# Kernel optimization log

Hardware: AMD Instinct MI355X
Metric: run time of the kernel (lower is better)

The kernel has to match this reference:

```python
import jax, jax.numpy as jnp
import numpy as np

L_XYZ = 10  # fourier freqs for position -> 3 + 6*10 = 63 dims
L_DIR = 4   # fourier freqs for direction -> 3 + 6*4 = 27 dims
DIM = 32    # radiance feature dim per depth layer
PPP = 4     # points (depth layers) per pixel
HID = 128   # MLP hidden width
UCH = 64    # UNet hidden channels


def pe(x, L):
    # fourier positional encoding: [x, sin(2^k x), cos(2^k x)]
    f = (2.0 ** jnp.arange(L)).astype(x.dtype)
    xf = x[..., None] * f  # [..., 3, L]
    s = jnp.sin(xf).reshape(x.shape[:-1] + (-1,))
    c = jnp.cos(xf).reshape(x.shape[:-1] + (-1,))
    return jnp.concatenate([x, s, c], axis=-1)


def conv(x, w, b):
    y = jax.lax.conv_general_dilated(x, w, (1, 1), 'SAME',
                                     dimension_numbers=('NCHW', 'OIHW', 'NCHW'))
    return y + b[None, :, None, None]


def setup_inputs() -> dict:
    key = jax.random.key(0)
    ks = jax.random.split(key, 24)
    H = W = 384
    zbufs = jax.random.uniform(ks[0], (H, W, PPP), dtype=jnp.float32)  # depths in [0,1)
    o = jax.random.normal(ks[1], (H, W, 3), dtype=jnp.float32)
    d = jax.random.normal(ks[2], (H, W, 3), dtype=jnp.float32)
    d = d / jnp.linalg.norm(d, axis=-1, keepdims=True)
    cos = jax.random.uniform(ks[3], (H, W, 1), dtype=jnp.float32) * 0.5 + 0.5
    ray = jnp.concatenate([o, d, cos], axis=-1)  # [H,W,7]
    gt = jax.random.uniform(ks[4], (H, W, 3), dtype=jnp.float32)
    mask_gt = jnp.ones((H, W, 1), dtype=jnp.float32)
    xyz_o = jax.random.normal(ks[5], (1024, 3), dtype=jnp.float32)
    in_xyz = 3 + 6 * L_XYZ
    in_dir = 3 + 6 * L_DIR
    in_ch = DIM * PPP
    p = {}
    p['w1'] = jax.random.normal(ks[6], (in_xyz, HID), dtype=jnp.float32) * 0.05
    p['b1'] = jnp.zeros((HID,), dtype=jnp.float32)
    p['w2'] = jax.random.normal(ks[7], (HID, HID), dtype=jnp.float32) * 0.05
    p['b2'] = jnp.zeros((HID,), dtype=jnp.float32)
    p['w3'] = jax.random.normal(ks[8], (HID + in_dir, DIM), dtype=jnp.float32) * 0.05
    p['b3'] = jnp.zeros((DIM,), dtype=jnp.float32)
    p['mpn_w1'] = jax.random.normal(ks[9], (in_ch, in_ch, 3, 3), dtype=jnp.float32) * 0.02
    p['mpn_b1'] = jnp.zeros((in_ch,), dtype=jnp.float32)
    p['mpn_w2'] = jax.random.normal(ks[10], (in_ch, in_ch, 3, 3), dtype=jnp.float32) * 0.02
    p['mpn_b2'] = jnp.zeros((in_ch,), dtype=jnp.float32)
    p['uw1'] = jax.random.normal(ks[11], (UCH, in_ch, 3, 3), dtype=jnp.float32) * 0.02
    p['ub1'] = jnp.zeros((UCH,), dtype=jnp.float32)
    p['uw2'] = jax.random.normal(ks[12], (UCH, UCH, 3, 3), dtype=jnp.float32) * 0.02
    p['ub2'] = jnp.zeros((UCH,), dtype=jnp.float32)
    p['uw3'] = jax.random.normal(ks[13], (3, UCH, 3, 3), dtype=jnp.float32) * 0.02
    p['ub3'] = jnp.zeros((3,), dtype=jnp.float32)
    inp = {'zbufs': zbufs, 'ray': ray, 'gt': gt, 'mask_gt': mask_gt,
           'isTrain': 1, 'xyz_o': xyz_o}
    inp.update(p)
    return inp


def reference(zbufs, ray, gt, mask_gt, isTrain, xyz_o,
              w1, b1, w2, b2, w3, b3,
              mpn_w1, mpn_b1, mpn_w2, mpn_b2,
              uw1, ub1, uw2, ub2, uw3, ub3):
    H, W, P = zbufs.shape
    o = ray[..., :3]
    dirs = ray[..., 3:6]
    cos = ray[..., 6:7]
    thresh = 0.2 if isTrain else 0.0
    # dense equivalent of boolean-mask gather -> MLP -> scatter into zeros
    mask = (zbufs > thresh).astype(zbufs.dtype)  # [H,W,P]
    # xyz_near = o + dirs * zbuf / cos  (xyznear path)
    xyz = o[..., None, :] + dirs[..., None, :] * zbufs[..., None] / cos[..., None]  # [H,W,P,3]
    x = pe(xyz, L_XYZ)                                   # [H,W,P,63]
    h = jax.nn.relu(x @ w1 + b1)                         # [H,W,P,HID]
    h = jax.nn.relu(h @ w2 + b2)
    dpe = pe(dirs, L_DIR)                                # [H,W,27]
    dpe = jnp.broadcast_to(dpe[..., None, :], h.shape[:-1] + (dpe.shape[-1],))
    feat = jnp.concatenate([h, dpe], axis=-1) @ w3 + b3  # [H,W,P,DIM]
    feat = feat * mask[..., None]                        # zeros where pix_mask is False
    # per-layer permute(2,3,0,1) + cat(dim=1) == [1, P*DIM, H, W]
    rdmp = feat.transpose(2, 3, 0, 1).reshape(1, P * DIM, H, W)
    # MPN: predicted per-channel mask
    m = jax.nn.sigmoid(conv(jax.nn.relu(conv(rdmp, mpn_w1, mpn_b1)), mpn_w2, mpn_b2))
    fuse = rdmp * m
    fea_map = jax.nn.sigmoid(fuse[0, :3].transpose(1, 2, 0))  # [H,W,3]
    # UNet refinement to RGB
    u = jax.nn.relu(conv(fuse, uw1, ub1))
    u = jax.nn.relu(conv(u, uw2, ub2))
    img = jax.nn.sigmoid(conv(u, uw3, ub3))[0].transpose(1, 2, 0)  # [H,W,3]
    return img
```

## Files before the change

kernel.cpp:

```cpp
#include <hip/hip_runtime.h>
#include <hip/hip_bf16.h>
#include <math.h>

typedef __attribute__((ext_vector_type(8))) unsigned short ushort8;
typedef __attribute__((ext_vector_type(8))) __bf16 bf16x8;
typedef __attribute__((ext_vector_type(4))) float floatx4;

constexpr int IMGW = 384;
constexpr int NPIX = IMGW * IMGW;

__device__ __forceinline__ unsigned short f2bf(float f) {
  union { float f; unsigned u; } v; v.f = f;
  unsigned u = v.u;
  return (unsigned short)((u + 0x7fffu + ((u >> 16) & 1u)) >> 16);
}
__device__ __forceinline__ float bf2f(unsigned short h) {
  union { unsigned u; float f; } v; v.u = ((unsigned)h) << 16; return v.f;
}
__device__ __forceinline__ unsigned pk2bf(float a, float b) {
  float2 f2; f2.x = a; f2.y = b;
  __hip_bfloat162 h = __float22bfloat162_rn(f2);
  union { __hip_bfloat162 h; unsigned u; } u; u.h = h; return u.u;
}
__device__ __forceinline__ floatx4 mfma16(bf16x8 a, bf16x8 b, floatx4 c) {
  return __builtin_amdgcn_mfma_f32_16x16x32_bf16(a, b, c, 0, 0, 0);
}
__device__ __forceinline__ bf16x8 lds_frag(const unsigned short* p) {
  return *reinterpret_cast<const bf16x8*>(p);
}
__device__ __forceinline__ bf16x8 u4_to_bf(uint4 v) {
  union { uint4 u; bf16x8 b; } c; c.u = v; return c.b;
}

__device__ __forceinline__ void convB_elem(const float* __restrict__ w,
                                           unsigned short* __restrict__ wt,
                                           int i, int CIN, int G, int NT) {
  int j = i & 7, lane = (i >> 3) & 63;
  int rest = i >> 9;
  int nt = rest % NT; int rest2 = rest / NT;
  int g = rest2 % G;  int ks = rest2 / G;
  int q = lane >> 4, m = lane & 15;
  int co = (g * NT + nt) * 16 + m;
  int k = ks * 32 + q * 8 + j;
  int nb = k / CIN, ci = k - nb * CIN;
  wt[i] = f2bf(w[(co * CIN + ci) * 9 + nb]);
}

__global__ __launch_bounds__(256) void prep_all(
    const float* __restrict__ w1, const float* __restrict__ w2, const float* __restrict__ w3,
    const float* __restrict__ mw1, const float* __restrict__ mw2,
    const float* __restrict__ uw1, const float* __restrict__ uw2,
    unsigned short* __restrict__ w1A, unsigned short* __restrict__ w2A,
    unsigned short* __restrict__ w3A,
    unsigned short* __restrict__ cw1, unsigned short* __restrict__ cw2,
    unsigned short* __restrict__ cu1, unsigned short* __restrict__ cu2) {
  int i = blockIdx.x * 256 + threadIdx.x;
  if (i < 28672) {
    if (i < 8192) {
      int j = i & 7, lane = (i >> 3) & 63, t = i >> 9;
      int mt = t >> 1, ks = t & 1;
      int ch_out = mt * 16 + (lane & 15);
      int kp = ks * 32 + (lane >> 4) * 8 + j;
      int chunk = kp >> 3, sl = kp & 7;
      float val;
      if (chunk == 7 && sl >= 4) {
        int c = sl - 4;
        val = (c < 3) ? w1[c * 128 + ch_out] : 0.0f;
      } else {
        const int coordA[8] = {0,0,0,1,1,2,2,2};
        const int octA[8]   = {0,4,8,2,6,0,4,8};
        const int coordB[8] = {0,0,1,1,1,2,2,2};
        const int octB[8]   = {2,6,0,4,8,2,6,0};
        int rc  = (sl < 4) ? coordA[chunk] : coordB[chunk];
        int oct = ((sl < 4) ? octA[chunk] : octB[chunk]) + ((sl >> 1) & 1);
        int korig = ((sl & 1) ? 33 : 3) + rc * 10 + oct;
        val = w1[korig * 128 + ch_out];
      }
      w1A[i] = f2bf(val);
    } else if (i < 24576) {
      int i2 = i - 8192;
      int j = i2 & 7, lane = (i2 >> 3) & 63, t = i2 >> 9;
      int mt = t >> 2, ks = t & 3;
      int ch_out = mt * 16 + (lane & 15);
      int kp = ks * 32 + (lane >> 4) * 8 + j;
      int c_orig = ((kp >> 2) & 7) * 16 + (kp >> 5) * 4 + (kp & 3);
      w2A[i2] = f2bf(w2[c_orig * 128 + ch_out]);
    } else {
      int i3 = i - 24576;
      int j = i3 & 7, lane = (i3 >> 3) & 63, t = i3 >> 9;
      int mt = t >> 2, ks = t & 3;
      int ch_out = mt * 16 + (lane & 15);
      int kp = ks * 32 + (lane >> 4) * 8 + j;
      int c_orig = ((kp >> 2) & 7) * 16 + (kp >> 5) * 4 + (kp & 3);
      w3A[i3] = f2bf(w3[c_orig * 32 + ch_out]);
    }
    return;
  }
  i -= 28672;
  if (i < 147456) { convB_elem(mw1, cw1, i, 128, 4, 2); return; }
  i -= 147456;
  if (i < 147456) { convB_elem(mw2, cw2, i, 128, 4, 2); return; }
  i -= 147456;
  if (i < 73728)  { convB_elem(uw1, cu1, i, 128, 4, 1); return; }
  i -= 73728;
  if (i < 36864)  { convB_elem(uw2, cu2, i, 64, 4, 1); return; }
}

__global__ __launch_bounds__(256) void dcon_kernel(
    const float* __restrict__ ray, const float* __restrict__ w3,
    const float* __restrict__ b3, float* __restrict__ dconG) {
  int gid = blockIdx.x * 256 + threadIdx.x;
  int pixel = gid >> 5, c = gid & 31;
  const float* r = ray + (size_t)pixel * 7;
  float d0 = r[3], d1 = r[4], d2 = r[5];
  float acc = b3[c];
  acc += d0 * w3[128 * 32 + c] + d1 * w3[129 * 32 + c] + d2 * w3[130 * 32 + c];
  float dv[3] = { d0, d1, d2 };
  #pragma unroll
  for (int cc = 0; cc < 3; ++cc) {
    float fs = 1.0f;
    #pragma unroll
    for (int f = 0; f < 4; ++f) {
      float s, co;
      __sincosf(dv[cc] * fs, &s, &co);
      acc += s * w3[(131 + cc * 4 + f) * 32 + c];
      acc += co * w3[(143 + cc * 4 + f) * 32 + c];
      fs *= 2.0f;
    }
  }
  dconG[gid] = acc;
}

__global__ __launch_bounds__(128, 4) void mlp_kernel(
    const float* __restrict__ zbufs, const float* __restrict__ ray,
    const int* __restrict__ isTrain,
    const float* __restrict__ b1, const float* __restrict__ b2,
    const unsigned short* __restrict__ w1A, const unsigned short* __restrict__ w2A,
    const unsigned short* __restrict__ w3A, const float* __restrict__ dconG,
    unsigned short* __restrict__ rdmp) {
  __shared__ __align__(16) unsigned short H[64 * 136];

  const int tid = threadIdx.x;
  const int half = tid >> 6;
  const int lane = tid & 63;
  const int q = lane >> 4, m = lane & 15;
  const float thresh = (isTrain[0] != 0) ? 0.2f : 0.0f;

  float fA[2], fB[2];
  int cAi[2], cBi[2];
  #pragma unroll
  for (int ks = 0; ks < 2; ++ks) {
    int ch = ks * 4 + q;
    cAi[ks] = (ch <= 2) ? 0 : ((ch <= 4) ? 1 : 2);
    fA[ks]  = (ch == 0 || ch == 5) ? 1.0f :
              (ch == 1 || ch == 6) ? 16.0f :
              (ch == 2 || ch == 7) ? 256.0f :
              (ch == 3) ? 4.0f : 64.0f;
    cBi[ks] = (ch <= 1) ? 0 : ((ch <= 4) ? 1 : 2);
    fB[ks]  = (ch == 2) ? 1.0f :
              (ch == 0 || ch == 5) ? 4.0f :
              (ch == 3) ? 16.0f :
              (ch == 1 || ch == 6) ? 64.0f : 256.0f;
  }

  bf16x8 bx[4][2];
  float zs[4];
  #pragma unroll
  for (int nt = 0; nt < 4; ++nt) {
    int s = nt * 16 + m;
    int sg = blockIdx.x * 64 + s;
    int pixel = sg >> 2;
    float z = zbufs[sg];
    zs[nt] = z;
    const float* r = ray + (size_t)pixel * 7;
    float t = z / r[6];
    float xv0 = r[0] + r[3] * t, xv1 = r[1] + r[4] * t, xv2 = r[2] + r[5] * t;
    #pragma unroll
    for (int ks = 0; ks < 2; ++ks) {
      float uA = (cAi[ks] == 0) ? xv0 : ((cAi[ks] == 1) ? xv1 : xv2);
      float uB = (cBi[ks] == 0) ? xv0 : ((cBi[ks] == 1) ? xv1 : xv2);
      float sa, ca, sb, cb;
      __sincosf(uA * fA[ks], &sa, &ca);
      __sincosf(uB * fB[ks], &sb, &cb);
      float t2a = sa + sa;
      float sa1 = t2a * ca, ca1 = fmaf(-t2a, sa, 1.0f);
      float t2b = sb + sb;
      float sb1 = t2b * cb, cb1 = fmaf(-t2b, sb, 1.0f);
      if (ks == 1 && q == 3) { sb = xv0; cb = xv1; sb1 = xv2; cb1 = 0.0f; }
      uint4 dv;
      dv.x = pk2bf(sa, ca); dv.y = pk2bf(sa1, ca1);
      dv.z = pk2bf(sb, cb); dv.w = pk2bf(sb1, cb1);
      bx[nt][ks] = u4_to_bf(dv);
    }
  }
  float zL[2];
  zL[0] = (half == 0) ? zs[0] : zs[2];
  zL[1] = (half == 0) ? zs[1] : zs[3];

  {
    floatx4 acc[4][4];
    #pragma unroll
    for (int mt = 0; mt < 4; ++mt) {
      float4 bb = *reinterpret_cast<const float4*>(b1 + (half * 4 + mt) * 16 + q * 4);
      #pragma unroll
      for (int nt = 0; nt < 4; ++nt) {
        acc[mt][nt][0] = bb.x; acc[mt][nt][1] = bb.y;
        acc[mt][nt][2] = bb.z; acc[mt][nt][3] = bb.w;
      }
    }
    #pragma unroll
    for (int ks = 0; ks < 2; ++ks) {
      #pragma unroll
      for (int mt = 0; mt < 4; ++mt) {
        int mtg = half * 4 + mt;
        bf16x8 a = *reinterpret_cast<const bf16x8*>(w1A + (((mtg << 1) + ks) << 9) + lane * 8);
        #pragma unroll
        for (int nt = 0; nt < 4; ++nt)
          acc[mt][nt] = mfma16(a, bx[nt][ks], acc[mt][nt]);
      }
    }
    #pragma unroll
    for (int nt = 0; nt < 4; ++nt) {
      uint4* base = reinterpret_cast<uint4*>(&H[(nt * 16 + m) * 136 + q * 32 + half * 16]);
      #pragma unroll
      for (int g = 0; g < 2; ++g) {
        uint4 v;
        v.x = pk2bf(fmaxf(acc[2*g][nt][0], 0.0f),   fmaxf(acc[2*g][nt][1], 0.0f));
        v.y = pk2bf(fmaxf(acc[2*g][nt][2], 0.0f),   fmaxf(acc[2*g][nt][3], 0.0f));
        v.z = pk2bf(fmaxf(acc[2*g+1][nt][0], 0.0f), fmaxf(acc[2*g+1][nt][1], 0.0f));
        v.w = pk2bf(fmaxf(acc[2*g+1][nt][2], 0.0f), fmaxf(acc[2*g+1][nt][3], 0.0f));
        base[g] = v;
      }
    }
  }
  __syncthreads();

  {
    uint4 keep[4][2];
    {
      floatx4 acc[4][4];
      #pragma unroll
      for (int mt = 0; mt < 4; ++mt) {
        float4 bb = *reinterpret_cast<const float4*>(b2 + (half * 4 + mt) * 16 + q * 4);
        #pragma unroll
        for (int nt = 0; nt < 4; ++nt) {
          acc[mt][nt][0] = bb.x; acc[mt][nt][1] = bb.y;
          acc[mt][nt][2] = bb.z; acc[mt][nt][3] = bb.w;
        }
      }
      #pragma unroll 1
      for (int ks = 0; ks < 4; ++ks) {
        bf16x8 bf[4];
        #pragma unroll
        for (int nt = 0; nt < 4; ++nt)
          bf[nt] = lds_frag(H + (nt * 16 + m) * 136 + ks * 32 + q * 8);
        #pragma unroll
        for (int mt = 0; mt < 4; ++mt) {
          int mtg = half * 4 + mt;
          bf16x8 a = *reinterpret_cast<const bf16x8*>(w2A + (((mtg << 2) + ks) << 9) + lane * 8);
          #pragma unroll
          for (int nt = 0; nt < 4; ++nt)
            acc[mt][nt] = mfma16(a, bf[nt], acc[mt][nt]);
        }
      }
      #pragma unroll
      for (int nt = 0; nt < 4; ++nt) {
        #pragma unroll
        for (int g = 0; g < 2; ++g) {
          uint4 v;
          v.x = pk2bf(fmaxf(acc[2*g][nt][0], 0.0f),   fmaxf(acc[2*g][nt][1], 0.0f));
          v.y = pk2bf(fmaxf(acc[2*g][nt][2], 0.0f),   fmaxf(acc[2*g][nt][3], 0.0f));
          v.z = pk2bf(fmaxf(acc[2*g+1][nt][0], 0.0f), fmaxf(acc[2*g+1][nt][1], 0.0f));
          v.w = pk2bf(fmaxf(acc[2*g+1][nt][2], 0.0f), fmaxf(acc[2*g+1][nt][3], 0.0f));
          keep[nt][g] = v;
        }
      }
    }
    __syncthreads();
    #pragma unroll
    for (int nt = 0; nt < 4; ++nt)
      #pragma unroll
      for (int g = 0; g < 2; ++g)
        *reinterpret_cast<uint4*>(&H[(nt * 16 + m) * 136 + q * 32 + half * 16 + g * 8]) = keep[nt][g];
  }
  __syncthreads();

  {
    floatx4 acc[2][2];
    const float* dg = dconG + (size_t)blockIdx.x * 512;
    #pragma unroll
    for (int nt2 = 0; nt2 < 2; ++nt2) {
      int s = (half * 2 + nt2) * 16 + m;
      #pragma unroll
      for (int mt = 0; mt < 2; ++mt)
        acc[mt][nt2] = *reinterpret_cast<const floatx4*>(dg + (s >> 2) * 32 + mt * 16 + q * 4);
    }
    #pragma unroll 2
    for (int ks = 0; ks < 4; ++ks) {
      bf16x8 bf[2];
      #pragma unroll
      for (int nt2 = 0; nt2 < 2; ++nt2)
        bf[nt2] = lds_frag(H + ((half * 2 + nt2) * 16 + m) * 136 + ks * 32 + q * 8);
      #pragma unroll
      for (int mt = 0; mt < 2; ++mt) {
        bf16x8 a = *reinterpret_cast<const bf16x8*>(w3A + (((mt << 2) + ks) << 9) + lane * 8);
        #pragma unroll
        for (int nt2 = 0; nt2 < 2; ++nt2)
          acc[mt][nt2] = mfma16(a, bf[nt2], acc[mt][nt2]);
      }
    }
    #pragma unroll
    for (int nt2 = 0; nt2 < 2; ++nt2) {
      int s = (half * 2 + nt2) * 16 + m;
      float mk = (zL[nt2] > thresh) ? 1.0f : 0.0f;
      unsigned short* dst = rdmp + (size_t)blockIdx.x * 2048 + s * 32 + q * 4;
      #pragma unroll
      for (int mt = 0; mt < 2; ++mt) {
        uint2 pk;
        pk.x = pk2bf(acc[mt][nt2][0] * mk, acc[mt][nt2][1] * mk);
        pk.y = pk2bf(acc[mt][nt2][2] * mk, acc[mt][nt2][3] * mk);
        *reinterpret_cast<uint2*>(dst + mt * 16) = pk;
      }
    }
  }
}

template<int CIN, int COUT, int MODE, int MINW>
__global__ __launch_bounds__(512, MINW) void conv3x3(
    const unsigned short* __restrict__ in, const unsigned short* __restrict__ wt,
    const float* __restrict__ bias, const unsigned short* __restrict__ rdmp,
    unsigned short* __restrict__ out) {
  constexpr int CP  = CIN + 8;
  constexpr int CH8 = CIN / 8;
  constexpr int KC  = CIN / 32;
  constexpr int NT  = COUT / 64;
  constexpr int GROUPS = KC * 3;
  __shared__ __align__(16) unsigned short lds_in[10 * 18 * CP];

  const int tid = threadIdx.x;
  const int x0 = blockIdx.x * 16, y0 = blockIdx.y * 8;

  for (int i = tid; i < 180 * CH8; i += 512) {
    int pix = i / CH8, part = i - pix * CH8;
    int xx = pix % 18, yy = pix / 18;
    int gx = x0 - 1 + xx, gy = y0 - 1 + yy;
    ushort8 v = {0, 0, 0, 0, 0, 0, 0, 0};
    if (gx >= 0 && gx < IMGW && gy >= 0 && gy < IMGW)
      v = *reinterpret_cast<const ushort8*>(in + ((size_t)(gy * IMGW + gx)) * CIN + part * 8);
    *reinterpret_cast<ushort8*>(&lds_in[pix * CP + part * 8]) = v;
  }
  __syncthreads();

  const int wave = tid >> 6, lane = tid & 63, q = lane >> 4, m = lane & 15;
  const int cw = wave & 3;
  const int rw = wave >> 2;
  floatx4 acc[4][NT] = {};

  auto loadB = [&](int g, bf16x8 (&bb)[3][NT]) {
    int kc = g / 3, dx = g - kc * 3;
    #pragma unroll
    for (int dy = 0; dy < 3; ++dy) {
      int ks = (dy * 3 + dx) * KC + kc;
      #pragma unroll
      for (int nt = 0; nt < NT; ++nt)
        bb[dy][nt] = *reinterpret_cast<const bf16x8*>(
            wt + ((((size_t)ks * 4 + cw) * NT + nt) << 9) + lane * 8);
    }
  };
  auto compute = [&](int g, bf16x8 (&bb)[3][NT]) {
    int kc = g / 3, dx = g - kc * 3;
    bf16x8 a[6];
    #pragma unroll
    for (int rr = 0; rr < 6; ++rr)
      a[rr] = lds_frag(&lds_in[((rw * 4 + rr) * 18 + m + dx) * CP + kc * 32 + q * 8]);
    #pragma unroll
    for (int dy = 0; dy < 3; ++dy)
      #pragma unroll
      for (int nt = 0; nt < NT; ++nt)
        #pragma unroll
        for (int mt = 0; mt < 4; ++mt)
          acc[mt][nt] = mfma16(a[mt + dy], bb[dy][nt], acc[mt][nt]);
  };

  bf16x8 b0[3][NT], b1[3][NT];
  loadB(0, b0);
  #pragma unroll 1
  for (int g = 0; g < GROUPS; g += 2) {
    loadB(g + 1, b1);
    compute(g, b0);
    if (g + 2 < GROUPS) loadB(g + 2, b0);
    compute(g + 1, b1);
  }

  const int co0 = cw * (COUT / 4);
  #pragma unroll
  for (int mt = 0; mt < 4; ++mt) {
    int y = y0 + rw * 4 + mt;
    #pragma unroll
    for (int nt = 0; nt < NT; ++nt) {
      int co = co0 + nt * 16 + m;
      float bb = bias[co];
      #pragma unroll
      for (int r = 0; r < 4; ++r) {
        int pixel = y * IMGW + x0 + q * 4 + r;
        float v = acc[mt][nt][r] + bb;
        if (MODE == 0) {
          v = fmaxf(v, 0.0f);
        } else {
          v = 1.0f / (1.0f + __expf(-v));
          v *= bf2f(rdmp[(size_t)pixel * 128 + co]);
        }
        out[(size_t)pixel * COUT + co] = f2bf(v);
      }
    }
  }
}

__global__ __launch_bounds__(256) void uconv3_kernel(
    const unsigned short* __restrict__ u2, const float* __restrict__ w,
    const float* __restrict__ b, float* __restrict__ out) {
  __shared__ float wl[1728];
  for (int i = threadIdx.x; i < 1728; i += 256) {
    int c = i % 3; int t = i / 3; int ci = t & 63; int nb = t >> 6;
    wl[i] = w[(c * 64 + ci) * 9 + nb];
  }
  __syncthreads();
  int pixel = blockIdx.x * 256 + threadIdx.x;
  int py = pixel / IMGW, px = pixel - py * IMGW;
  float a0 = b[0], a1 = b[1], a2 = b[2];
  for (int nb = 0; nb < 9; ++nb) {
    int gy = py + nb / 3 - 1, gx = px + nb % 3 - 1;
    if (gx < 0 || gx >= IMGW || gy < 0 || gy >= IMGW) continue;
    const unsigned short* src = u2 + (size_t)(gy * IMGW + gx) * 64;
    const float* wp = wl + nb * 192;
    #pragma unroll
    for (int cc = 0; cc < 8; ++cc) {
      ushort8 v = *reinterpret_cast<const ushort8*>(src + cc * 8);
      #pragma unroll
      for (int j = 0; j < 8; ++j) {
        float uv = bf2f(v[j]);
        const float* w3p = wp + (cc * 8 + j) * 3;
        a0 += uv * w3p[0]; a1 += uv * w3p[1]; a2 += uv * w3p[2];
      }
    }
  }
  float* o = out + (size_t)pixel * 3;
  o[0] = 1.0f / (1.0f + __expf(-a0));
  o[1] = 1.0f / (1.0f + __expf(-a1));
  o[2] = 1.0f / (1.0f + __expf(-a2));
}

extern "C" void kernel_launch(void* const* d_in, const int* in_sizes, int n_in,
                              void* d_out, int out_size, void* d_ws, size_t ws_size,
                              hipStream_t stream) {
  (void)in_sizes; (void)n_in; (void)out_size; (void)ws_size;
  const float* zbufs = (const float*)d_in[0];
  const float* ray   = (const float*)d_in[1];
  const int* isTrain = (const int*)d_in[4];
  const float* w1 = (const float*)d_in[6];
  const float* b1 = (const float*)d_in[7];
  const float* w2 = (const float*)d_in[8];
  const float* b2 = (const float*)d_in[9];
  const float* w3 = (const float*)d_in[10];
  const float* b3 = (const float*)d_in[11];
  const float* mpn_w1 = (const float*)d_in[12];
  const float* mpn_b1 = (const float*)d_in[13];
  const float* mpn_w2 = (const float*)d_in[14];
  const float* mpn_b2 = (const float*)d_in[15];
  const float* uw1 = (const float*)d_in[16];
  const float* ub1 = (const float*)d_in[17];
  const float* uw2 = (const float*)d_in[18];
  const float* ub2 = (const float*)d_in[19];
  const float* uw3 = (const float*)d_in[20];
  const float* ub3 = (const float*)d_in[21];
  float* out = (float*)d_out;

  unsigned char* ws = (unsigned char*)d_ws;
  size_t off = 0;
  auto alloc = [&](size_t bytes) -> void* {
    void* p = ws + off; off = (off + bytes + 255) & ~(size_t)255; return p;
  };
  unsigned short* w1A  = (unsigned short*)alloc(8192 * 2);
  unsigned short* w2A  = (unsigned short*)alloc(16384 * 2);
  unsigned short* w3A  = (unsigned short*)alloc(4096 * 2);
  unsigned short* cw1  = (unsigned short*)alloc((size_t)128 * 1152 * 2);
  unsigned short* cw2  = (unsigned short*)alloc((size_t)128 * 1152 * 2);
  unsigned short* cu1  = (unsigned short*)alloc((size_t)64 * 1152 * 2);
  unsigned short* cu2  = (unsigned short*)alloc((size_t)64 * 576 * 2);
  unsigned short* rdmp = (unsigned short*)alloc((size_t)NPIX * 128 * 2);
  unsigned short* t1   = (unsigned short*)alloc((size_t)NPIX * 128 * 2);
  unsigned short* fuse = (unsigned short*)alloc((size_t)NPIX * 128 * 2);
  unsigned short* u1 = t1;
  unsigned short* u2 = rdmp;
  float* dconG = (float*)fuse;

  prep_all<<<1696, 256, 0, stream>>>(w1, w2, w3, mpn_w1, mpn_w2, uw1, uw2,
                                     w1A, w2A, w3A, cw1, cw2, cu1, cu2);
  dcon_kernel<<<NPIX * 32 / 256, 256, 0, stream>>>(ray, w3, b3, dconG);
  mlp_kernel<<<NPIX * 4 / 64, 128, 0, stream>>>(zbufs, ray, isTrain, b1, b2,
                                                w1A, w2A, w3A, dconG, rdmp);

  dim3 cgrid(IMGW / 16, IMGW / 8);
  conv3x3<128, 128, 0, 4><<<cgrid, 512, 0, stream>>>(rdmp, cw1, mpn_b1, nullptr, t1);
  conv3x3<128, 128, 1, 4><<<cgrid, 512, 0, stream>>>(t1, cw2, mpn_b2, rdmp, fuse);
  conv3x3<128, 64, 0, 4><<<cgrid, 512, 0, stream>>>(fuse, cu1, ub1, nullptr, u1);
  conv3x3<64, 64, 0, 4><<<cgrid, 512, 0, stream>>>(u1, cu2, ub2, nullptr, u2);
  uconv3_kernel<<<NPIX / 256, 256, 0, stream>>>(u2, uw3, ub3, out);
}
```

Baseline: 356.6 us.

## Fold direction encoding into MLP via MFMA and move final conv to MFMA

Removes the separate direction-encoding kernel and its global buffer. The direction positional encoding is now computed inside the MLP kernel and applied as an extra MFMA k-step, using an extended w3A layout built in prep. The final 64->3 conv is also rewritten to use bf16 MFMA over an LDS-staged 18x10 halo tile instead of scalar FP32 per-pixel loops. This saves one launch and a per-pixel 32-float write/read. In exchange it adds sincos work to the MLP kernel and pads the output conv to 16 channels, of which only 3 are used.

```diff
diff --git a/kernel.cpp b/kernel.cpp
--- a/kernel.cpp
+++ b/kernel.cpp
@@ -50,12 +50,14 @@
     const float* __restrict__ w1, const float* __restrict__ w2, const float* __restrict__ w3,
     const float* __restrict__ mw1, const float* __restrict__ mw2,
     const float* __restrict__ uw1, const float* __restrict__ uw2,
+    const float* __restrict__ uw3,
     unsigned short* __restrict__ w1A, unsigned short* __restrict__ w2A,
     unsigned short* __restrict__ w3A,
     unsigned short* __restrict__ cw1, unsigned short* __restrict__ cw2,
-    unsigned short* __restrict__ cu1, unsigned short* __restrict__ cu2) {
+    unsigned short* __restrict__ cu1, unsigned short* __restrict__ cu2,
+    unsigned short* __restrict__ cu3) {
   int i = blockIdx.x * 256 + threadIdx.x;
-  if (i < 28672) {
+  if (i < 29696) {
     if (i < 8192) {
       int j = i & 7, lane = (i >> 3) & 63, t = i >> 9;
       int mt = t >> 1, ks = t & 1;
@@ -88,15 +90,33 @@
     } else {
       int i3 = i - 24576;
       int j = i3 & 7, lane = (i3 >> 3) & 63, t = i3 >> 9;
-      int mt = t >> 2, ks = t & 3;
-      int ch_out = mt * 16 + (lane & 15);
-      int kp = ks * 32 + (lane >> 4) * 8 + j;
-      int c_orig = ((kp >> 2) & 7) * 16 + (kp >> 5) * 4 + (kp & 3);
-      w3A[i3] = f2bf(w3[c_orig * 32 + ch_out]);
+      int mt = (t >= 5) ? 1 : 0; int ks = t - mt * 5;
+      int q = lane >> 4, m = lane & 15;
+      int ch_out = mt * 16 + m;
+      float val;
+      if (ks < 4) {
+        int kp = ks * 32 + q * 8 + j;
+        int c_orig = ((kp >> 2) & 7) * 16 + (kp >> 5) * 4 + (kp & 3);
+        val = w3[c_orig * 32 + ch_out];
+      } else {
+        int row = -1;
+        if (q == 0) {
+          if (j < 3) row = 128 + j;
+          else if (j >= 4) {
+            int ga = (j - 4) >> 1;
+            row = (((j - 4) & 1) == 0 ? 131 : 143) + ga;
+          }
+        } else {
+          int ga = q * 4 - 2 + (j >> 1);
+          if (ga < 12) row = ((j & 1) == 0 ? 131 : 143) + ga;
+        }
+        val = (row >= 0) ? w3[row * 32 + ch_out] : 0.0f;
+      }
+      w3A[(((mt << 3) + ks) << 9) + (lane << 3) + j] = f2bf(val);
     }
     return;
   }
-  i -= 28672;
+  i -= 29696;
   if (i < 147456) { convB_elem(mw1, cw1, i, 128, 4, 2); return; }
   i -= 147456;
   if (i < 147456) { convB_elem(mw2, cw2, i, 128, 4, 2); return; }
@@ -104,39 +124,24 @@
   if (i < 73728)  { convB_elem(uw1, cu1, i, 128, 4, 1); return; }
   i -= 73728;
   if (i < 36864)  { convB_elem(uw2, cu2, i, 64, 4, 1); return; }
-}
-
-__global__ __launch_bounds__(256) void dcon_kernel(
-    const float* __restrict__ ray, const float* __restrict__ w3,
-    const float* __restrict__ b3, float* __restrict__ dconG) {
-  int gid = blockIdx.x * 256 + threadIdx.x;
-  int pixel = gid >> 5, c = gid & 31;
-  const float* r = ray + (size_t)pixel * 7;
-  float d0 = r[3], d1 = r[4], d2 = r[5];
-  float acc = b3[c];
-  acc += d0 * w3[128 * 32 + c] + d1 * w3[129 * 32 + c] + d2 * w3[130 * 32 + c];
-  float dv[3] = { d0, d1, d2 };
-  #pragma unroll
-  for (int cc = 0; cc < 3; ++cc) {
-    float fs = 1.0f;
-    #pragma unroll
-    for (int f = 0; f < 4; ++f) {
-      float s, co;
-      __sincosf(dv[cc] * fs, &s, &co);
-      acc += s * w3[(131 + cc * 4 + f) * 32 + c];
-      acc += co * w3[(143 + cc * 4 + f) * 32 + c];
-      fs *= 2.0f;
-    }
-  }
-  dconG[gid] = acc;
+  i -= 36864;
+  {
+    int j = i & 7, lane = (i >> 3) & 63, ks = i >> 9;
+    int q = lane >> 4, m = lane & 15;
+    int k = ks * 32 + q * 8 + j;
+    int nb = k >> 6, ci = k & 63;
+    float val = (m < 3) ? uw3[(m * 64 + ci) * 9 + nb] : 0.0f;
+    cu3[i] = f2bf(val);
+  }
 }
 
 __global__ __launch_bounds__(128, 4) void mlp_kernel(
     const float* __restrict__ zbufs, const float* __restrict__ ray,
     const int* __restrict__ isTrain,
     const float* __restrict__ b1, const float* __restrict__ b2,
+    const float* __restrict__ b3,
     const unsigned short* __restrict__ w1A, const unsigned short* __restrict__ w2A,
-    const unsigned short* __restrict__ w3A, const float* __restrict__ dconG,
+    const unsigned short* __restrict__ w3A,
     unsigned short* __restrict__ rdmp) {
   __shared__ __align__(16) unsigned short H[64 * 136];
 
@@ -164,6 +169,7 @@
   }
 
   bf16x8 bx[4][2];
+  bf16x8 dpe0, dpe1;
   float zs[4];
   #pragma unroll
   for (int nt = 0; nt < 4; ++nt) {
@@ -192,6 +198,36 @@
       dv.z = pk2bf(sb, cb); dv.w = pk2bf(sb1, cb1);
       bx[nt][ks] = u4_to_bf(dv);
     }
+    if ((nt >> 1) == half) {
+      float dd0 = r[3], dd1 = r[4], dd2 = r[5];
+      float ss[4], cc[4];
+      #pragma unroll
+      for (int ii = 0; ii < 4; ++ii) {
+        int a = q * 4 + ii - 2;
+        int ac = (a < 0 || a > 11) ? 0 : a;
+        int c = ac >> 2;
+        float base = (c == 0) ? dd0 : ((c == 1) ? dd1 : dd2);
+        float fs = (float)(1 << (ac & 3));
+        __sincosf(base * fs, &ss[ii], &cc[ii]);
+      }
+      uint4 dv;
+      if (q == 0) {
+        dv.x = pk2bf(dd0, dd1);
+        dv.y = pk2bf(dd2, 0.0f);
+        dv.z = pk2bf(ss[2], cc[2]);
+        dv.w = pk2bf(ss[3], cc[3]);
+      } else if (q == 3) {
+        dv.x = pk2bf(ss[0], cc[0]);
+        dv.y = pk2bf(ss[1], cc[1]);
+        dv.z = 0u; dv.w = 0u;
+      } else {
+        dv.x = pk2bf(ss[0], cc[0]);
+        dv.y = pk2bf(ss[1], cc[1]);
+        dv.z = pk2bf(ss[2], cc[2]);
+        dv.w = pk2bf(ss[3], cc[3]);
+      }
+      if ((nt & 1) == 0) dpe0 = u4_to_bf(dv); else dpe1 = u4_to_bf(dv);
+    }
   }
   float zL[2];
   zL[0] = (half == 0) ? zs[0] : zs[2];
@@ -287,13 +323,20 @@
 
   {
     floatx4 acc[2][2];
-    const float* dg = dconG + (size_t)blockIdx.x * 512;
-    #pragma unroll
-    for (int nt2 = 0; nt2 < 2; ++nt2) {
-      int s = (half * 2 + nt2) * 16 + m;
-      #pragma unroll
-      for (int mt = 0; mt < 2; ++mt)
-        acc[mt][nt2] = *reinterpret_cast<const floatx4*>(dg + (s >> 2) * 32 + mt * 16 + q * 4);
+    #pragma unroll
+    for (int mt = 0; mt < 2; ++mt) {
+      float4 bb3 = *reinterpret_cast<const float4*>(b3 + mt * 16 + q * 4);
+      #pragma unroll
+      for (int nt2 = 0; nt2 < 2; ++nt2) {
+        acc[mt][nt2][0] = bb3.x; acc[mt][nt2][1] = bb3.y;
+        acc[mt][nt2][2] = bb3.z; acc[mt][nt2][3] = bb3.w;
+      }
+    }
+    #pragma unroll
+    for (int mt = 0; mt < 2; ++mt) {
+      bf16x8 a = *reinterpret_cast<const bf16x8*>(w3A + (((mt << 3) + 4) << 9) + lane * 8);
+      acc[mt][0] = mfma16(a, dpe0, acc[mt][0]);
+      acc[mt][1] = mfma16(a, dpe1, acc[mt][1]);
     }
     #pragma unroll 2
     for (int ks = 0; ks < 4; ++ks) {
@@ -303,7 +346,7 @@
         bf[nt2] = lds_frag(H + ((half * 2 + nt2) * 16 + m) * 136 + ks * 32 + q * 8);
       #pragma unroll
       for (int mt = 0; mt < 2; ++mt) {
-        bf16x8 a = *reinterpret_cast<const bf16x8*>(w3A + (((mt << 2) + ks) << 9) + lane * 8);
+        bf16x8 a = *reinterpret_cast<const bf16x8*>(w3A + (((mt << 3) + ks) << 9) + lane * 8);
         #pragma unroll
         for (int nt2 = 0; nt2 < 2; ++nt2)
           acc[mt][nt2] = mfma16(a, bf[nt2], acc[mt][nt2]);
@@ -417,37 +460,54 @@
 }
 
 __global__ __launch_bounds__(256) void uconv3_kernel(
-    const unsigned short* __restrict__ u2, const float* __restrict__ w,
+    const unsigned short* __restrict__ u2, const unsigned short* __restrict__ wt,
     const float* __restrict__ b, float* __restrict__ out) {
-  __shared__ float wl[1728];
-  for (int i = threadIdx.x; i < 1728; i += 256) {
-    int c = i % 3; int t = i / 3; int ci = t & 63; int nb = t >> 6;
-    wl[i] = w[(c * 64 + ci) * 9 + nb];
+  __shared__ __align__(16) unsigned short lds_in[180 * 72];
+  const int tid = threadIdx.x;
+  const int x0 = blockIdx.x * 16, y0 = blockIdx.y * 8;
+  for (int i = tid; i < 180 * 8; i += 256) {
+    int pix = i >> 3, part = i & 7;
+    int xx = pix % 18, yy = pix / 18;
+    int gx = x0 - 1 + xx, gy = y0 - 1 + yy;
+    ushort8 v = {0, 0, 0, 0, 0, 0, 0, 0};
+    if (gx >= 0 && gx < IMGW && gy >= 0 && gy < IMGW)
+      v = *reinterpret_cast<const ushort8*>(u2 + (size_t)(gy * IMGW + gx) * 64 + part * 8);
+    *reinterpret_cast<ushort8*>(&lds_in[pix * 72 + part * 8]) = v;
   }
   __syncthreads();
-  int pixel = blockIdx.x * 256 + threadIdx.x;
-  int py = pixel / IMGW, px = pixel - py * IMGW;
-  float a0 = b[0], a1 = b[1], a2 = b[2];
-  for (int nb = 0; nb < 9; ++nb) {
-    int gy = py + nb / 3 - 1, gx = px + nb % 3 - 1;
-    if (gx < 0 || gx >= IMGW || gy < 0 || gy >= IMGW) continue;
-    const unsigned short* src = u2 + (size_t)(gy * IMGW + gx) * 64;
-    const float* wp = wl + nb * 192;
-    #pragma unroll
-    for (int cc = 0; cc < 8; ++cc) {
-      ushort8 v = *reinterpret_cast<const ushort8*>(src + cc * 8);
-      #pragma unroll
-      for (int j = 0; j < 8; ++j) {
-        float uv = bf2f(v[j]);
-        const float* w3p = wp + (cc * 8 + j) * 3;
-        a0 += uv * w3p[0]; a1 += uv * w3p[1]; a2 += uv * w3p[2];
-      }
-    }
-  }
-  float* o = out + (size_t)pixel * 3;
-  o[0] = 1.0f / (1.0f + __expf(-a0));
-  o[1] = 1.0f / (1.0f + __expf(-a1));
-  o[2] = 1.0f / (1.0f + __expf(-a2));
+  const int wave = tid >> 6, lane = tid & 63, q = lane >> 4, m = lane & 15;
+  floatx4 acc[2] = {};
+  #pragma unroll 1
+  for (int g = 0; g < 6; ++g) {
+    int kc = g / 3, dx = g - kc * 3;
+    bf16x8 bb[3];
+    #pragma unroll
+    for (int dy = 0; dy < 3; ++dy) {
+      int ks = (dy * 3 + dx) * 2 + kc;
+      bb[dy] = *reinterpret_cast<const bf16x8*>(wt + (ks << 9) + lane * 8);
+    }
+    bf16x8 a[4];
+    #pragma unroll
+    for (int rr = 0; rr < 4; ++rr)
+      a[rr] = lds_frag(&lds_in[((wave * 2 + rr) * 18 + m + dx) * 72 + kc * 32 + q * 8]);
+    #pragma unroll
+    for (int dy = 0; dy < 3; ++dy)
+      #pragma unroll
+      for (int mt = 0; mt < 2; ++mt)
+        acc[mt] = mfma16(a[mt + dy], bb[dy], acc[mt]);
+  }
+  if (m < 3) {
+    float bbv = b[m];
+    #pragma unroll
+    for (int mt = 0; mt < 2; ++mt) {
+      int y = y0 + wave * 2 + mt;
+      #pragma unroll
+      for (int r = 0; r < 4; ++r) {
+        int pixel = y * IMGW + x0 + q * 4 + r;
+        out[(size_t)pixel * 3 + m] = 1.0f / (1.0f + __expf(-(acc[mt][r] + bbv)));
+      }
+    }
+  }
 }
 
 extern "C" void kernel_launch(void* const* d_in, const int* in_sizes, int n_in,
@@ -482,28 +542,27 @@
   };
   unsigned short* w1A  = (unsigned short*)alloc(8192 * 2);
   unsigned short* w2A  = (unsigned short*)alloc(16384 * 2);
-  unsigned short* w3A  = (unsigned short*)alloc(4096 * 2);
+  unsigned short* w3A  = (unsigned short*)alloc(8192 * 2);
   unsigned short* cw1  = (unsigned short*)alloc((size_t)128 * 1152 * 2);
   unsigned short* cw2  = (unsigned short*)alloc((size_t)128 * 1152 * 2);
   unsigned short* cu1  = (unsigned short*)alloc((size_t)64 * 1152 * 2);
   unsigned short* cu2  = (unsigned short*)alloc((size_t)64 * 576 * 2);
+  unsigned short* cu3  = (unsigned short*)alloc((size_t)9216 * 2);
   unsigned short* rdmp = (unsigned short*)alloc((size_t)NPIX * 128 * 2);
   unsigned short* t1   = (unsigned short*)alloc((size_t)NPIX * 128 * 2);
   unsigned short* fuse = (unsigned short*)alloc((size_t)NPIX * 128 * 2);
   unsigned short* u1 = t1;
   unsigned short* u2 = rdmp;
-  float* dconG = (float*)fuse;
-
-  prep_all<<<1696, 256, 0, stream>>>(w1, w2, w3, mpn_w1, mpn_w2, uw1, uw2,
-                                     w1A, w2A, w3A, cw1, cw2, cu1, cu2);
-  dcon_kernel<<<NPIX * 32 / 256, 256, 0, stream>>>(ray, w3, b3, dconG);
-  mlp_kernel<<<NPIX * 4 / 64, 128, 0, stream>>>(zbufs, ray, isTrain, b1, b2,
-                                                w1A, w2A, w3A, dconG, rdmp);
+
+  prep_all<<<1736, 256, 0, stream>>>(w1, w2, w3, mpn_w1, mpn_w2, uw1, uw2, uw3,
+                                     w1A, w2A, w3A, cw1, cw2, cu1, cu2, cu3);
+  mlp_kernel<<<NPIX * 4 / 64, 128, 0, stream>>>(zbufs, ray, isTrain, b1, b2, b3,
+                                                w1A, w2A, w3A, rdmp);
 
   dim3 cgrid(IMGW / 16, IMGW / 8);
   conv3x3<128, 128, 0, 4><<<cgrid, 512, 0, stream>>>(rdmp, cw1, mpn_b1, nullptr, t1);
   conv3x3<128, 128, 1, 4><<<cgrid, 512, 0, stream>>>(t1, cw2, mpn_b2, rdmp, fuse);
   conv3x3<128, 64, 0, 4><<<cgrid, 512, 0, stream>>>(fuse, cu1, ub1, nullptr, u1);
   conv3x3<64, 64, 0, 4><<<cgrid, 512, 0, stream>>>(u1, cu2, ub2, nullptr, u2);
-  uconv3_kernel<<<NPIX / 256, 256, 0, stream>>>(u2, uw3, ub3, out);
-}
+  uconv3_kernel<<<cgrid, 256, 0, stream>>>(u2, cu3, ub3, out);
+}
```

Result: faster. 304.6 us (-14.6%).
